# Performance work log

Measured on AMD Instinct MI355X. Metric: run time of the kernel, lower is better.

The kernel has to match this reference:

```python
import jax, jax.numpy as jnp
import numpy as np

N_NODES = 50000
N_EDGES = 800000
IN_DIM = 128
OUT_DIM = 128
NUM_RELS = 100
NUM_BASES = 4


def setup_inputs() -> dict:
    key = jax.random.key(0)
    ks = jax.random.split(key, 8)
    h = jax.random.normal(ks[0], (N_NODES, IN_DIM), dtype=jnp.float32)
    norm = jax.random.uniform(ks[1], (N_NODES, 1), dtype=jnp.float32)
    src = jax.random.randint(ks[2], (N_EDGES,), 0, N_NODES, dtype=jnp.int32)
    dst = jax.random.randint(ks[3], (N_EDGES,), 0, N_NODES, dtype=jnp.int32)
    rel_type = jax.random.randint(ks[4], (N_EDGES,), 0, NUM_RELS, dtype=jnp.int32)
    basis_weights = jax.random.normal(ks[5], (NUM_BASES, IN_DIM, OUT_DIM), dtype=jnp.float32) * (2.0 / np.sqrt(IN_DIM + OUT_DIM))
    coefficients = jax.random.normal(ks[6], (NUM_RELS, NUM_BASES), dtype=jnp.float32) * (1.0 / np.sqrt(NUM_RELS + NUM_BASES))
    loop_weight = jax.random.normal(ks[7], (IN_DIM, OUT_DIM), dtype=jnp.float32) * (2.0 / np.sqrt(IN_DIM + OUT_DIM))
    return {
        'h': h, 'norm': norm, 'src': src, 'dst': dst, 'rel_type': rel_type,
        'basis_weights': basis_weights, 'coefficients': coefficients,
        'loop_weight': loop_weight,
    }


def reference(h, norm, src, dst, rel_type, basis_weights, coefficients, loop_weight):
    # h: (N, in), norm: (N, 1), src/dst/rel_type: (E,)
    # basis_weights: (B, in, out), coefficients: (R, B), loop_weight: (in, out)
    n_nodes = h.shape[0]
    num_bases = basis_weights.shape[0]

    # self-loop message (dropout=0 -> identity)
    loop_message = h @ loop_weight  # (N, out)

    # W[r] = sum_b coeff[r, b] * basis[b]; per-edge msg_e = h[src_e] @ W[rel_e].
    # Reassociated: project nodes by each basis once, then mix per edge by
    # the relation coefficients -- identical math, avoids the (E, in, out)
    # gathered weight tensor of the original per-edge bmm.
    hb = jnp.einsum('ni,bio->bno', h, basis_weights)  # (B, N, out)
    c_e = coefficients[rel_type]  # (E, B)
    msg = c_e[:, 0, None] * hb[0][src]
    for b in range(1, num_bases):  # small fixed basis count
        msg = msg + c_e[:, b, None] * hb[b][src]  # (E, out)

    # scatter-sum aggregation to destination nodes, then norm scaling
    agg = jax.ops.segment_sum(msg, dst, num_segments=n_nodes)  # (N, out)
    node_repr = agg * norm  # _apply_func
    node_repr = node_repr + loop_message  # self-loop (bias=None)
    return jax.nn.relu(node_repr)  # activation
```

## Files before the change

### kernel.cpp

```cpp
#include <hip/hip_runtime.h>

typedef short bf16x8 __attribute__((ext_vector_type(8)));
typedef float floatx4 __attribute__((ext_vector_type(4)));
typedef float floatx2 __attribute__((ext_vector_type(2)));

typedef const __attribute__((address_space(1))) void* gas_ptr;
typedef __attribute__((address_space(3))) void* las_ptr;

#define EPB  4096
#define MAXB 6144

__device__ __forceinline__ unsigned short f2bf(float f) {
    unsigned int u = __float_as_uint(f);
    unsigned int r = u + 0x7fffu + ((u >> 16) & 1u);
    return (unsigned short)(r >> 16);
}

__device__ __forceinline__ void stage16(const void* g, void* lbase, int lane) {
#if __has_builtin(__builtin_amdgcn_global_load_lds)
    __builtin_amdgcn_global_load_lds((gas_ptr)g, (las_ptr)lbase, 16, 0, 0);
#else
    *(float4*)((char*)lbase + lane * 16) = *(const float4*)g;
#endif
}

__global__ __launch_bounds__(256) void prep_all(
    const float* __restrict__ h, unsigned short* __restrict__ hbf, int nconv,
    const int* __restrict__ dst, int* __restrict__ gh, int E, int nB, int nblkH,
    const float* __restrict__ basis, const float* __restrict__ loopw,
    unsigned short* __restrict__ WT2, int nb_conv)
{
    __shared__ int lh[256];
    const int b = blockIdx.x;
    const int t = threadIdx.x;
    if (b < nb_conv) {
        int idx = b * 256 + t;
        if (idx < nconv) {
            float2 v = *(const float2*)(h + (size_t)idx * 2);
            unsigned int pack = (unsigned int)f2bf(v.x) | ((unsigned int)f2bf(v.y) << 16);
            *(unsigned int*)(hbf + (size_t)idx * 2) = pack;
        }
    } else if (b < nb_conv + nblkH) {
        const int blk = b - nb_conv;
        if (t < nB) lh[t] = 0;
        __syncthreads();
        const int cbase = blk * EPB;
#pragma unroll
        for (int j = 0; j < EPB / 256; ++j) {
            int e = cbase + j * 256 + t;
            if (e < E) atomicAdd(&lh[dst[e] >> 8], 1);
        }
        __syncthreads();
        if (t < nB) gh[(size_t)t * nblkH + blk] = lh[t];
    } else {
        int c = b - nb_conv - nblkH;
        for (int k = t; k < 640; k += 256) {
            float v;
            if (k < 512) v = basis[(size_t)k * 128 + c];
            else         v = loopw[(size_t)(k - 512) * 128 + c];
            WT2[(size_t)c * 640 + k] = f2bf(v);
        }
    }
}

__global__ __launch_bounds__(256) void scan1(
    const int* __restrict__ in, int* __restrict__ bsum, int M)
{
    __shared__ int s[256];
    int i = blockIdx.x * 256 + threadIdx.x;
    int t = threadIdx.x;
    s[t] = (i < M) ? in[i] : 0;
    __syncthreads();
    for (int o = 128; o > 0; o >>= 1) {
        if (t < o) s[t] += s[t + o];
        __syncthreads();
    }
    if (t == 0) bsum[blockIdx.x] = s[0];
}

__global__ __launch_bounds__(256) void scan_final(
    const int* __restrict__ in, const int* __restrict__ bsum,
    int* __restrict__ out, int M)
{
    __shared__ int s[256];
    __shared__ int sb[256];
    int t = threadIdx.x;
    int i = blockIdx.x * 256 + t;
    sb[t] = (t < (int)blockIdx.x) ? bsum[t] : 0;
    int v = (i < M) ? in[i] : 0;
    s[t] = v;
    __syncthreads();
    for (int o = 128; o > 0; o >>= 1) {
        if (t < o) sb[t] += sb[t + o];
        __syncthreads();
    }
    for (int o = 1; o < 256; o <<= 1) {
        int x = (t >= o) ? s[t - o] : 0;
        __syncthreads();
        s[t] += x;
        __syncthreads();
    }
    if (i < M) out[i] = s[t] - v + sb[0];
}

__global__ __launch_bounds__(256) void scatter_bkt(
    const int* __restrict__ dst, const int* __restrict__ src,
    const int* __restrict__ rel, const int* __restrict__ sgh,
    unsigned int* __restrict__ tmp, int E, int nB, int nblkH)
{
    __shared__ int cur[256];
    const int blk = blockIdx.x;
    const int t = threadIdx.x;
    if (t < nB) cur[t] = sgh[(size_t)t * nblkH + blk];
    __syncthreads();
    const int cbase = blk * EPB;
#pragma unroll
    for (int j = 0; j < EPB / 256; ++j) {
        int e = cbase + j * 256 + t;
        if (e < E) {
            int d = dst[e];
            int slot = atomicAdd(&cur[d >> 8], 1);
            tmp[slot] = (unsigned int)src[e] | ((unsigned int)rel[e] << 16)
                      | ((unsigned int)(d & 255) << 23);
        }
    }
}

__global__ __launch_bounds__(256) void bucket_sort(
    const unsigned int* __restrict__ tmp, const int* __restrict__ sgh,
    unsigned int* __restrict__ sedge, int* __restrict__ rowptr,
    int E, int N, int nB, int nblkH)
{
    __shared__ unsigned int eb[MAXB];
    __shared__ int hh[256], ss[256], cur[256];
    const int b = blockIdx.x;
    const int t = threadIdx.x;
    const int brow = sgh[(size_t)b * nblkH];
    const int next = (b + 1 < nB) ? sgh[(size_t)(b + 1) * nblkH] : E;
    int n = next - brow;
    if (n > MAXB) n = MAXB;
    hh[t] = 0;
    __syncthreads();
    for (int i = t; i < n; i += 256) {
        unsigned int v = tmp[brow + i];
        eb[i] = v;
        atomicAdd(&hh[(v >> 23) & 255], 1);
    }
    __syncthreads();
    int v = hh[t];
    ss[t] = v;
    __syncthreads();
    for (int o = 1; o < 256; o <<= 1) {
        int x = (t >= o) ? ss[t - o] : 0;
        __syncthreads();
        ss[t] += x;
        __syncthreads();
    }
    const int excl = ss[t] - v;
    const int idx = b * 256 + t;
    if (idx <= N) rowptr[idx] = brow + excl;
    cur[t] = excl;
    __syncthreads();
    for (int i = t; i < n; i += 256) {
        unsigned int e = eb[i];
        int slot = atomicAdd(&cur[(e >> 23) & 255], 1);
        sedge[brow + slot] = ((e & 0xFFFFu) << 8) | (((e >> 16) & 0x7Fu) << 25);
    }
}

__global__ __launch_bounds__(256) void aggregate_pre(
    const unsigned short* __restrict__ hbf,
    const int* __restrict__ rowptr,
    const unsigned int* __restrict__ sedge,
    const float* __restrict__ coeff,
    const float* __restrict__ norm,
    unsigned short* __restrict__ A2, int N, int R)
{
    __shared__ float scoef[512];
    for (int i = threadIdx.x; i < R * 4; i += 256) scoef[i] = coeff[i];
    __syncthreads();

    const int wave = threadIdx.x >> 6;
    const int lane = threadIdx.x & 63;
    const int d = blockIdx.x * 4 + wave;
    if (d >= N) return;
    int i = rowptr[d];
    const int end = rowptr[d + 1];

    const char* hbase = (const char*)hbf + lane * 4;

    floatx2 a0 = {0.f, 0.f}, a1 = {0.f, 0.f}, a2 = {0.f, 0.f}, a3 = {0.f, 0.f};

#define EDGE_LOAD(v, u) \
    unsigned int u = *(const unsigned int*)(hbase + ((v) & 0x00FFFF00u));
#define EDGE_MATH(v, u) { \
    const float4 c = *(const float4*)((const char*)scoef + (((v) >> 25) << 4)); \
    floatx2 hp; \
    hp[0] = __uint_as_float((u) << 16); \
    hp[1] = __uint_as_float((u) & 0xFFFF0000u); \
    a0 = __builtin_elementwise_fma((floatx2){c.x, c.x}, hp, a0); \
    a1 = __builtin_elementwise_fma((floatx2){c.y, c.y}, hp, a1); \
    a2 = __builtin_elementwise_fma((floatx2){c.z, c.z}, hp, a2); \
    a3 = __builtin_elementwise_fma((floatx2){c.w, c.w}, hp, a3); }

    while (i < end && (i & 3)) {
        unsigned int v = sedge[i];
        EDGE_LOAD(v, u)
        EDGE_MATH(v, u)
        ++i;
    }
    for (; i + 8 <= end; i += 8) {
        uint4 e0 = *(const uint4*)(sedge + i);
        uint4 e1 = *(const uint4*)(sedge + i + 4);
        EDGE_LOAD(e0.x, u0) EDGE_LOAD(e0.y, u1) EDGE_LOAD(e0.z, u2) EDGE_LOAD(e0.w, u3)
        EDGE_LOAD(e1.x, u4) EDGE_LOAD(e1.y, u5) EDGE_LOAD(e1.z, u6) EDGE_LOAD(e1.w, u7)
        EDGE_MATH(e0.x, u0) EDGE_MATH(e0.y, u1) EDGE_MATH(e0.z, u2) EDGE_MATH(e0.w, u3)
        EDGE_MATH(e1.x, u4) EDGE_MATH(e1.y, u5) EDGE_MATH(e1.z, u6) EDGE_MATH(e1.w, u7)
    }
    for (; i + 4 <= end; i += 4) {
        uint4 e0 = *(const uint4*)(sedge + i);
        EDGE_LOAD(e0.x, u0) EDGE_LOAD(e0.y, u1) EDGE_LOAD(e0.z, u2) EDGE_LOAD(e0.w, u3)
        EDGE_MATH(e0.x, u0) EDGE_MATH(e0.y, u1) EDGE_MATH(e0.z, u2) EDGE_MATH(e0.w, u3)
    }
    for (; i < end; ++i) {
        unsigned int v = sedge[i];
        EDGE_LOAD(v, u)
        EDGE_MATH(v, u)
    }
#undef EDGE_LOAD
#undef EDGE_MATH

    const float nm = norm[d];
    unsigned short* row = A2 + (size_t)d * 512 + lane * 2;
    *(unsigned int*)(row)       = (unsigned int)f2bf(a0[0] * nm) | ((unsigned int)f2bf(a0[1] * nm) << 16);
    *(unsigned int*)(row + 128) = (unsigned int)f2bf(a1[0] * nm) | ((unsigned int)f2bf(a1[1] * nm) << 16);
    *(unsigned int*)(row + 256) = (unsigned int)f2bf(a2[0] * nm) | ((unsigned int)f2bf(a2[1] * nm) << 16);
    *(unsigned int*)(row + 384) = (unsigned int)f2bf(a3[0] * nm) | ((unsigned int)f2bf(a3[1] * nm) << 16);
}

__global__ __launch_bounds__(256) void final_gemm(
    const unsigned short* __restrict__ A2,
    const unsigned short* __restrict__ hbf,
    const unsigned short* __restrict__ WT2,
    float* __restrict__ out, int N)
{
    __shared__ char sA[16384];
    __shared__ char sB[16384];
    const int t = threadIdx.x;
    const int w = t >> 6;
    const int lane = t & 63;
    const int quad = lane >> 4;
    const int low  = lane & 15;
    const int wr = w >> 1, wc = w & 1;
    const int m0 = blockIdx.x * 128;

    floatx4 acc[4][4];
#pragma unroll
    for (int mt = 0; mt < 4; ++mt)
#pragma unroll
        for (int nt = 0; nt < 4; ++nt) acc[mt][nt] = (floatx4){0.f, 0.f, 0.f, 0.f};

    for (int it = 0; it < 10; ++it) {
        const int k0 = it * 64;
#pragma unroll
        for (int i = 0; i < 4; ++i) {
            const int slot = i * 256 + t;
            const int kc  = slot >> 7;
            const int idx = slot & 127;
            int grow = m0 + idx;
            if (grow >= N) grow = N - 1;
            const unsigned short* gA = (k0 < 512)
                ? A2  + (size_t)grow * 512 + k0 + kc * 8
                : hbf + (size_t)grow * 128 + (k0 - 512) + kc * 8;
            const unsigned short* gB = WT2 + (size_t)idx * 640 + k0 + kc * 8;
            stage16(gA, sA + (size_t)(i * 256 + w * 64) * 16, lane);
            stage16(gB, sB + (size_t)(i * 256 + w * 64) * 16, lane);
        }
        __syncthreads();

#pragma unroll
        for (int ks = 0; ks < 2; ++ks) {
            bf16x8 af[4], bfr[4];
#pragma unroll
            for (int mt = 0; mt < 4; ++mt)
                af[mt] = *(const bf16x8*)(sA + (size_t)(((ks * 4 + quad) << 7) + wr * 64 + mt * 16 + low) * 16);
#pragma unroll
            for (int nt = 0; nt < 4; ++nt)
                bfr[nt] = *(const bf16x8*)(sB + (size_t)(((ks * 4 + quad) << 7) + wc * 64 + nt * 16 + low) * 16);
#pragma unroll
            for (int mt = 0; mt < 4; ++mt)
#pragma unroll
                for (int nt = 0; nt < 4; ++nt)
                    acc[mt][nt] = __builtin_amdgcn_mfma_f32_16x16x32_bf16(af[mt], bfr[nt], acc[mt][nt], 0, 0, 0);
        }
        __syncthreads();
    }

#pragma unroll
    for (int mt = 0; mt < 4; ++mt) {
#pragma unroll
        for (int nt = 0; nt < 4; ++nt) {
            const int c = wc * 64 + nt * 16 + low;
#pragma unroll
            for (int r = 0; r < 4; ++r) {
                int rr = m0 + wr * 64 + mt * 16 + quad * 4 + r;
                if (rr < N) out[(size_t)rr * 128 + c] = fmaxf(acc[mt][nt][r], 0.f);
            }
        }
    }
}

extern "C" void kernel_launch(void* const* d_in, const int* in_sizes, int n_in,
                              void* d_out, int out_size, void* d_ws, size_t ws_size,
                              hipStream_t stream)
{
    const float* h     = (const float*)d_in[0];
    const float* norm  = (const float*)d_in[1];
    const int*   src   = (const int*)d_in[2];
    const int*   dst   = (const int*)d_in[3];
    const int*   rel   = (const int*)d_in[4];
    const float* basis = (const float*)d_in[5];
    const float* coeff = (const float*)d_in[6];
    const float* loopw = (const float*)d_in[7];
    float* out = (float*)d_out;

    const int N = in_sizes[1];
    const int E = in_sizes[2];
    const int R = in_sizes[6] / 4;

    const int nB    = (N + 255) >> 8;
    const int nblkH = (E + EPB - 1) / EPB;
    const int M     = nB * nblkH;
    const int NBs   = (M + 255) / 256;

    char* ws = (char*)d_ws;
    size_t off = 0;
    auto walloc = [&](size_t bytes) -> char* {
        char* p = ws + off;
        off = (off + bytes + 255) & ~(size_t)255;
        return p;
    };
    unsigned short* A2     = (unsigned short*)walloc((size_t)N * 512 * 2);
    unsigned short* hbf    = (unsigned short*)walloc((size_t)N * 128 * 2);
    unsigned short* WT2    = (unsigned short*)walloc(128 * 640 * 2);
    int*            rowptr = (int*)walloc((size_t)(N + 1) * 4);
    int*            bsum   = (int*)walloc((size_t)NBs * 4);
    int*            gh     = (int*)walloc((size_t)M * 4);
    int*            sgh    = (int*)walloc((size_t)M * 4);
    unsigned int*   tmp    = (unsigned int*)walloc((size_t)E * 4);
    unsigned int*   sedge  = (unsigned int*)walloc((size_t)E * 4);

    const int nconv = N * 64;
    const int nb_conv = (nconv + 255) / 256;

    prep_all<<<nb_conv + nblkH + 128, 256, 0, stream>>>(
        h, hbf, nconv, dst, gh, E, nB, nblkH, basis, loopw, WT2, nb_conv);
    scan1<<<NBs, 256, 0, stream>>>(gh, bsum, M);
    scan_final<<<NBs, 256, 0, stream>>>(gh, bsum, sgh, M);
    scatter_bkt<<<nblkH, 256, 0, stream>>>(dst, src, rel, sgh, tmp, E, nB, nblkH);
    bucket_sort<<<nB, 256, 0, stream>>>(tmp, sgh, sedge, rowptr, E, N, nB, nblkH);
    aggregate_pre<<<(N + 3) / 4, 256, 0, stream>>>(hbf, rowptr, sedge, coeff, norm, A2, N, R);
    final_gemm<<<(N + 127) / 128, 256, 0, stream>>>(A2, hbf, WT2, out, N);
}
```

Before: 202.1 us.

## Fuse edge aggregation with final GEMM through a swizzled LDS tile

Result: slower. 231.4 us (+14.5%).

```diff
diff --git a/kernel.cpp b/kernel.cpp
--- a/kernel.cpp
+++ b/kernel.cpp
@@ -3,9 +3,6 @@
 typedef short bf16x8 __attribute__((ext_vector_type(8)));
 typedef float floatx4 __attribute__((ext_vector_type(4)));
 typedef float floatx2 __attribute__((ext_vector_type(2)));
-
-typedef const __attribute__((address_space(1))) void* gas_ptr;
-typedef __attribute__((address_space(3))) void* las_ptr;
 
 #define EPB  4096
 #define MAXB 6144
@@ -14,14 +11,6 @@
     unsigned int u = __float_as_uint(f);
     unsigned int r = u + 0x7fffu + ((u >> 16) & 1u);
     return (unsigned short)(r >> 16);
-}
-
-__device__ __forceinline__ void stage16(const void* g, void* lbase, int lane) {
-#if __has_builtin(__builtin_amdgcn_global_load_lds)
-    __builtin_amdgcn_global_load_lds((gas_ptr)g, (las_ptr)lbase, 16, 0, 0);
-#else
-    *(float4*)((char*)lbase + lane * 16) = *(const float4*)g;
-#endif
 }
 
 __global__ __launch_bounds__(256) void prep_all(
@@ -168,28 +157,27 @@
     }
 }
 
-__global__ __launch_bounds__(256) void aggregate_pre(
+__global__ __launch_bounds__(256, 4) void agg_gemm(
     const unsigned short* __restrict__ hbf,
     const int* __restrict__ rowptr,
     const unsigned int* __restrict__ sedge,
     const float* __restrict__ coeff,
     const float* __restrict__ norm,
-    unsigned short* __restrict__ A2, int N, int R)
-{
+    const unsigned short* __restrict__ WT2,
+    float* __restrict__ out, int N, int R)
+{
+    __shared__ unsigned short sA[64 * 32 * 8];
     __shared__ float scoef[512];
-    for (int i = threadIdx.x; i < R * 4; i += 256) scoef[i] = coeff[i];
-    __syncthreads();
-
-    const int wave = threadIdx.x >> 6;
-    const int lane = threadIdx.x & 63;
-    const int d = blockIdx.x * 4 + wave;
-    if (d >= N) return;
-    int i = rowptr[d];
-    const int end = rowptr[d + 1];
+
+    const int t = threadIdx.x;
+    for (int i = t; i < R * 4; i += 256) scoef[i] = coeff[i];
+    __syncthreads();
+
+    const int wave = t >> 6;
+    const int lane = t & 63;
+    const int m0 = blockIdx.x * 32;
 
     const char* hbase = (const char*)hbf + lane * 4;
-
-    floatx2 a0 = {0.f, 0.f}, a1 = {0.f, 0.f}, a2 = {0.f, 0.f}, a3 = {0.f, 0.f};
 
 #define EDGE_LOAD(v, u) \
     unsigned int u = *(const unsigned int*)(hbase + ((v) & 0x00FFFF00u));
@@ -198,113 +186,125 @@
     floatx2 hp; \
     hp[0] = __uint_as_float((u) << 16); \
     hp[1] = __uint_as_float((u) & 0xFFFF0000u); \
-    a0 = __builtin_elementwise_fma((floatx2){c.x, c.x}, hp, a0); \
-    a1 = __builtin_elementwise_fma((floatx2){c.y, c.y}, hp, a1); \
-    a2 = __builtin_elementwise_fma((floatx2){c.z, c.z}, hp, a2); \
-    a3 = __builtin_elementwise_fma((floatx2){c.w, c.w}, hp, a3); }
-
-    while (i < end && (i & 3)) {
-        unsigned int v = sedge[i];
-        EDGE_LOAD(v, u)
-        EDGE_MATH(v, u)
-        ++i;
-    }
-    for (; i + 8 <= end; i += 8) {
-        uint4 e0 = *(const uint4*)(sedge + i);
-        uint4 e1 = *(const uint4*)(sedge + i + 4);
-        EDGE_LOAD(e0.x, u0) EDGE_LOAD(e0.y, u1) EDGE_LOAD(e0.z, u2) EDGE_LOAD(e0.w, u3)
-        EDGE_LOAD(e1.x, u4) EDGE_LOAD(e1.y, u5) EDGE_LOAD(e1.z, u6) EDGE_LOAD(e1.w, u7)
-        EDGE_MATH(e0.x, u0) EDGE_MATH(e0.y, u1) EDGE_MATH(e0.z, u2) EDGE_MATH(e0.w, u3)
-        EDGE_MATH(e1.x, u4) EDGE_MATH(e1.y, u5) EDGE_MATH(e1.z, u6) EDGE_MATH(e1.w, u7)
-    }
-    for (; i + 4 <= end; i += 4) {
-        uint4 e0 = *(const uint4*)(sedge + i);
-        EDGE_LOAD(e0.x, u0) EDGE_LOAD(e0.y, u1) EDGE_LOAD(e0.z, u2) EDGE_LOAD(e0.w, u3)
-        EDGE_MATH(e0.x, u0) EDGE_MATH(e0.y, u1) EDGE_MATH(e0.z, u2) EDGE_MATH(e0.w, u3)
-    }
-    for (; i < end; ++i) {
-        unsigned int v = sedge[i];
-        EDGE_LOAD(v, u)
-        EDGE_MATH(v, u)
+    a[0] = __builtin_elementwise_fma((floatx2){c.x, c.x}, hp, a[0]); \
+    a[1] = __builtin_elementwise_fma((floatx2){c.y, c.y}, hp, a[1]); \
+    a[2] = __builtin_elementwise_fma((floatx2){c.z, c.z}, hp, a[2]); \
+    a[3] = __builtin_elementwise_fma((floatx2){c.w, c.w}, hp, a[3]); }
+
+    for (int j = 0; j < 8; ++j) {
+        const int r = wave * 8 + j;
+        const int d = m0 + r;
+        if (d >= N) break;
+        int i = rowptr[d];
+        const int end = rowptr[d + 1];
+
+        floatx2 a[4];
+        a[0] = (floatx2){0.f, 0.f}; a[1] = (floatx2){0.f, 0.f};
+        a[2] = (floatx2){0.f, 0.f}; a[3] = (floatx2){0.f, 0.f};
+
+        while (i < end && (i & 3)) {
+            unsigned int v = sedge[i];
+            EDGE_LOAD(v, u)
+            EDGE_MATH(v, u)
+            ++i;
+        }
+        for (; i + 8 <= end; i += 8) {
+            uint4 e0 = *(const uint4*)(sedge + i);
+            uint4 e1 = *(const uint4*)(sedge + i + 4);
+            EDGE_LOAD(e0.x, u0) EDGE_LOAD(e0.y, u1) EDGE_LOAD(e0.z, u2) EDGE_LOAD(e0.w, u3)
+            EDGE_LOAD(e1.x, u4) EDGE_LOAD(e1.y, u5) EDGE_LOAD(e1.z, u6) EDGE_LOAD(e1.w, u7)
+            EDGE_MATH(e0.x, u0) EDGE_MATH(e0.y, u1) EDGE_MATH(e0.z, u2) EDGE_MATH(e0.w, u3)
+            EDGE_MATH(e1.x, u4) EDGE_MATH(e1.y, u5) EDGE_MATH(e1.z, u6) EDGE_MATH(e1.w, u7)
+        }
+        for (; i + 4 <= end; i += 4) {
+            uint4 e0 = *(const uint4*)(sedge + i);
+            EDGE_LOAD(e0.x, u0) EDGE_LOAD(e0.y, u1) EDGE_LOAD(e0.z, u2) EDGE_LOAD(e0.w, u3)
+            EDGE_MATH(e0.x, u0) EDGE_MATH(e0.y, u1) EDGE_MATH(e0.z, u2) EDGE_MATH(e0.w, u3)
+        }
+        for (; i < end; ++i) {
+            unsigned int v = sedge[i];
+            EDGE_LOAD(v, u)
+            EDGE_MATH(v, u)
+        }
+
+        const float nm = norm[d];
+        const int kbase = lane >> 2;
+        const int boff = (lane & 3) * 4;
+#pragma unroll
+        for (int b = 0; b < 4; ++b) {
+            unsigned int pack = (unsigned int)f2bf(a[b][0] * nm)
+                              | ((unsigned int)f2bf(a[b][1] * nm) << 16);
+            const int kc = b * 16 + kbase;
+            const int slot = kc * 32 + (r ^ (kc & 7));
+            *(unsigned int*)((char*)sA + (size_t)slot * 16 + boff) = pack;
+        }
     }
 #undef EDGE_LOAD
 #undef EDGE_MATH
 
-    const float nm = norm[d];
-    unsigned short* row = A2 + (size_t)d * 512 + lane * 2;
-    *(unsigned int*)(row)       = (unsigned int)f2bf(a0[0] * nm) | ((unsigned int)f2bf(a0[1] * nm) << 16);
-    *(unsigned int*)(row + 128) = (unsigned int)f2bf(a1[0] * nm) | ((unsigned int)f2bf(a1[1] * nm) << 16);
-    *(unsigned int*)(row + 256) = (unsigned int)f2bf(a2[0] * nm) | ((unsigned int)f2bf(a2[1] * nm) << 16);
-    *(unsigned int*)(row + 384) = (unsigned int)f2bf(a3[0] * nm) | ((unsigned int)f2bf(a3[1] * nm) << 16);
-}
-
-__global__ __launch_bounds__(256) void final_gemm(
-    const unsigned short* __restrict__ A2,
-    const unsigned short* __restrict__ hbf,
-    const unsigned short* __restrict__ WT2,
-    float* __restrict__ out, int N)
-{
-    __shared__ char sA[16384];
-    __shared__ char sB[16384];
-    const int t = threadIdx.x;
-    const int w = t >> 6;
-    const int lane = t & 63;
+    __syncthreads();
+
     const int quad = lane >> 4;
     const int low  = lane & 15;
-    const int wr = w >> 1, wc = w & 1;
-    const int m0 = blockIdx.x * 128;
-
-    floatx4 acc[4][4];
-#pragma unroll
-    for (int mt = 0; mt < 4; ++mt)
-#pragma unroll
-        for (int nt = 0; nt < 4; ++nt) acc[mt][nt] = (floatx4){0.f, 0.f, 0.f, 0.f};
-
-    for (int it = 0; it < 10; ++it) {
-        const int k0 = it * 64;
-#pragma unroll
-        for (int i = 0; i < 4; ++i) {
-            const int slot = i * 256 + t;
-            const int kc  = slot >> 7;
-            const int idx = slot & 127;
-            int grow = m0 + idx;
-            if (grow >= N) grow = N - 1;
-            const unsigned short* gA = (k0 < 512)
-                ? A2  + (size_t)grow * 512 + k0 + kc * 8
-                : hbf + (size_t)grow * 128 + (k0 - 512) + kc * 8;
-            const unsigned short* gB = WT2 + (size_t)idx * 640 + k0 + kc * 8;
-            stage16(gA, sA + (size_t)(i * 256 + w * 64) * 16, lane);
-            stage16(gB, sB + (size_t)(i * 256 + w * 64) * 16, lane);
-        }
-        __syncthreads();
-
-#pragma unroll
-        for (int ks = 0; ks < 2; ++ks) {
-            bf16x8 af[4], bfr[4];
-#pragma unroll
-            for (int mt = 0; mt < 4; ++mt)
-                af[mt] = *(const bf16x8*)(sA + (size_t)(((ks * 4 + quad) << 7) + wr * 64 + mt * 16 + low) * 16);
-#pragma unroll
-            for (int nt = 0; nt < 4; ++nt)
-                bfr[nt] = *(const bf16x8*)(sB + (size_t)(((ks * 4 + quad) << 7) + wc * 64 + nt * 16 + low) * 16);
-#pragma unroll
-            for (int mt = 0; mt < 4; ++mt)
-#pragma unroll
-                for (int nt = 0; nt < 4; ++nt)
-                    acc[mt][nt] = __builtin_amdgcn_mfma_f32_16x16x32_bf16(af[mt], bfr[nt], acc[mt][nt], 0, 0, 0);
-        }
-        __syncthreads();
-    }
-
-#pragma unroll
-    for (int mt = 0; mt < 4; ++mt) {
-#pragma unroll
-        for (int nt = 0; nt < 4; ++nt) {
-            const int c = wc * 64 + nt * 16 + low;
-#pragma unroll
-            for (int r = 0; r < 4; ++r) {
-                int rr = m0 + wr * 64 + mt * 16 + quad * 4 + r;
-                if (rr < N) out[(size_t)rr * 128 + c] = fmaxf(acc[mt][nt][r], 0.f);
+
+    floatx4 acc[2][2];
+#pragma unroll
+    for (int mt = 0; mt < 2; ++mt)
+#pragma unroll
+        for (int nt = 0; nt < 2; ++nt) acc[mt][nt] = (floatx4){0.f, 0.f, 0.f, 0.f};
+
+#pragma unroll 4
+    for (int kk = 0; kk < 16; ++kk) {
+        const int kcq = kk * 4 + quad;
+        bf16x8 af[2], bfr[2];
+#pragma unroll
+        for (int mt = 0; mt < 2; ++mt) {
+            const int row = mt * 16 + low;
+            af[mt] = *(const bf16x8*)((const char*)sA
+                        + (size_t)(kcq * 32 + (row ^ (kcq & 7))) * 16);
+        }
+#pragma unroll
+        for (int nt = 0; nt < 2; ++nt) {
+            const int col = wave * 32 + nt * 16 + low;
+            bfr[nt] = *(const bf16x8*)(WT2 + (size_t)col * 640 + kk * 32 + quad * 8);
+        }
+#pragma unroll
+        for (int mt = 0; mt < 2; ++mt)
+#pragma unroll
+            for (int nt = 0; nt < 2; ++nt)
+                acc[mt][nt] = __builtin_amdgcn_mfma_f32_16x16x32_bf16(af[mt], bfr[nt], acc[mt][nt], 0, 0, 0);
+    }
+
+#pragma unroll
+    for (int kk = 16; kk < 20; ++kk) {
+        bf16x8 af[2], bfr[2];
+#pragma unroll
+        for (int mt = 0; mt < 2; ++mt) {
+            int rowd = m0 + mt * 16 + low;
+            if (rowd >= N) rowd = N - 1;
+            af[mt] = *(const bf16x8*)(hbf + (size_t)rowd * 128 + (kk - 16) * 32 + quad * 8);
+        }
+#pragma unroll
+        for (int nt = 0; nt < 2; ++nt) {
+            const int col = wave * 32 + nt * 16 + low;
+            bfr[nt] = *(const bf16x8*)(WT2 + (size_t)col * 640 + kk * 32 + quad * 8);
+        }
+#pragma unroll
+        for (int mt = 0; mt < 2; ++mt)
+#pragma unroll
+            for (int nt = 0; nt < 2; ++nt)
+                acc[mt][nt] = __builtin_amdgcn_mfma_f32_16x16x32_bf16(af[mt], bfr[nt], acc[mt][nt], 0, 0, 0);
+    }
+
+#pragma unroll
+    for (int mt = 0; mt < 2; ++mt) {
+#pragma unroll
+        for (int nt = 0; nt < 2; ++nt) {
+            const int c = wave * 32 + nt * 16 + low;
+#pragma unroll
+            for (int r2 = 0; r2 < 4; ++r2) {
+                int rr = m0 + mt * 16 + quad * 4 + r2;
+                if (rr < N) out[(size_t)rr * 128 + c] = fmaxf(acc[mt][nt][r2], 0.f);
             }
         }
     }
@@ -340,7 +340,6 @@
         off = (off + bytes + 255) & ~(size_t)255;
         return p;
     };
-    unsigned short* A2     = (unsigned short*)walloc((size_t)N * 512 * 2);
     unsigned short* hbf    = (unsigned short*)walloc((size_t)N * 128 * 2);
     unsigned short* WT2    = (unsigned short*)walloc(128 * 640 * 2);
     int*            rowptr = (int*)walloc((size_t)(N + 1) * 4);
@@ -359,6 +358,5 @@
     scan_final<<<NBs, 256, 0, stream>>>(gh, bsum, sgh, M);
     scatter_bkt<<<nblkH, 256, 0, stream>>>(dst, src, rel, sgh, tmp, E, nB, nblkH);
     bucket_sort<<<nB, 256, 0, stream>>>(tmp, sgh, sedge, rowptr, E, N, nB, nblkH);
-    aggregate_pre<<<(N + 3) / 4, 256, 0, stream>>>(hbf, rowptr, sedge, coeff, norm, A2, N, R);
-    final_gemm<<<(N + 127) / 128, 256, 0, stream>>>(A2, hbf, WT2, out, N);
-}
+    agg_gemm<<<(N + 31) / 32, 256, 0, stream>>>(hbf, rowptr, sedge, coeff, norm, WT2, out, N, R);
+}
```

## Replace bucketed two-pass CSR sort with direct global-atomic counting sort

Applied to the files above, without the earlier changes.

Result: slower. 259.3 us (+28.3%).

```diff
diff --git a/kernel.cpp b/kernel.cpp
--- a/kernel.cpp
+++ b/kernel.cpp
@@ -6,9 +6,6 @@
 
 typedef const __attribute__((address_space(1))) void* gas_ptr;
 typedef __attribute__((address_space(3))) void* las_ptr;
-
-#define EPB  4096
-#define MAXB 6144
 
 __device__ __forceinline__ unsigned short f2bf(float f) {
     unsigned int u = __float_as_uint(f);
@@ -25,35 +22,35 @@
 }
 
 __global__ __launch_bounds__(256) void prep_all(
-    const float* __restrict__ h, unsigned short* __restrict__ hbf, int nconv,
-    const int* __restrict__ dst, int* __restrict__ gh, int E, int nB, int nblkH,
+    const float* __restrict__ h, unsigned short* __restrict__ hbf, int nconv8,
+    const int* __restrict__ dst, int* __restrict__ cnt, int E, int nhist,
     const float* __restrict__ basis, const float* __restrict__ loopw,
     unsigned short* __restrict__ WT2, int nb_conv)
 {
-    __shared__ int lh[256];
     const int b = blockIdx.x;
     const int t = threadIdx.x;
     if (b < nb_conv) {
         int idx = b * 256 + t;
-        if (idx < nconv) {
-            float2 v = *(const float2*)(h + (size_t)idx * 2);
-            unsigned int pack = (unsigned int)f2bf(v.x) | ((unsigned int)f2bf(v.y) << 16);
-            *(unsigned int*)(hbf + (size_t)idx * 2) = pack;
-        }
-    } else if (b < nb_conv + nblkH) {
+        if (idx < nconv8) {
+            const float4 v0 = *(const float4*)(h + (size_t)idx * 8);
+            const float4 v1 = *(const float4*)(h + (size_t)idx * 8 + 4);
+            uint4 p;
+            p.x = (unsigned int)f2bf(v0.x) | ((unsigned int)f2bf(v0.y) << 16);
+            p.y = (unsigned int)f2bf(v0.z) | ((unsigned int)f2bf(v0.w) << 16);
+            p.z = (unsigned int)f2bf(v1.x) | ((unsigned int)f2bf(v1.y) << 16);
+            p.w = (unsigned int)f2bf(v1.z) | ((unsigned int)f2bf(v1.w) << 16);
+            *(uint4*)(hbf + (size_t)idx * 8) = p;
+        }
+    } else if (b < nb_conv + nhist) {
         const int blk = b - nb_conv;
-        if (t < nB) lh[t] = 0;
-        __syncthreads();
-        const int cbase = blk * EPB;
-#pragma unroll
-        for (int j = 0; j < EPB / 256; ++j) {
+        const int cbase = blk * 2048;
+#pragma unroll
+        for (int j = 0; j < 8; ++j) {
             int e = cbase + j * 256 + t;
-            if (e < E) atomicAdd(&lh[dst[e] >> 8], 1);
-        }
-        __syncthreads();
-        if (t < nB) gh[(size_t)t * nblkH + blk] = lh[t];
+            if (e < E) atomicAdd(&cnt[dst[e]], 1);
+        }
     } else {
-        int c = b - nb_conv - nblkH;
+        int c = b - nb_conv - nhist;
         for (int k = t; k < 640; k += 256) {
             float v;
             if (k < 512) v = basis[(size_t)k * 128 + c];
@@ -80,7 +77,7 @@
 
 __global__ __launch_bounds__(256) void scan_final(
     const int* __restrict__ in, const int* __restrict__ bsum,
-    int* __restrict__ out, int M)
+    int* __restrict__ rowptr, int* __restrict__ gcur, int M, int E)
 {
     __shared__ int s[256];
     __shared__ int sb[256];
@@ -100,71 +97,29 @@
         s[t] += x;
         __syncthreads();
     }
-    if (i < M) out[i] = s[t] - v + sb[0];
-}
-
-__global__ __launch_bounds__(256) void scatter_bkt(
+    if (i < M) {
+        int excl = s[t] - v + sb[0];
+        rowptr[i] = excl;
+        gcur[i]   = excl;
+    }
+    if (blockIdx.x == 0 && t == 0) rowptr[M] = E;
+}
+
+__global__ __launch_bounds__(256) void scatter_direct(
     const int* __restrict__ dst, const int* __restrict__ src,
-    const int* __restrict__ rel, const int* __restrict__ sgh,
-    unsigned int* __restrict__ tmp, int E, int nB, int nblkH)
-{
-    __shared__ int cur[256];
-    const int blk = blockIdx.x;
+    const int* __restrict__ rel, int* __restrict__ gcur,
+    unsigned int* __restrict__ sedge, int E)
+{
+    const int cbase = blockIdx.x * 2048;
     const int t = threadIdx.x;
-    if (t < nB) cur[t] = sgh[(size_t)t * nblkH + blk];
-    __syncthreads();
-    const int cbase = blk * EPB;
-#pragma unroll
-    for (int j = 0; j < EPB / 256; ++j) {
+#pragma unroll
+    for (int j = 0; j < 8; ++j) {
         int e = cbase + j * 256 + t;
         if (e < E) {
             int d = dst[e];
-            int slot = atomicAdd(&cur[d >> 8], 1);
-            tmp[slot] = (unsigned int)src[e] | ((unsigned int)rel[e] << 16)
-                      | ((unsigned int)(d & 255) << 23);
-        }
-    }
-}
-
-__global__ __launch_bounds__(256) void bucket_sort(
-    const unsigned int* __restrict__ tmp, const int* __restrict__ sgh,
-    unsigned int* __restrict__ sedge, int* __restrict__ rowptr,
-    int E, int N, int nB, int nblkH)
-{
-    __shared__ unsigned int eb[MAXB];
-    __shared__ int hh[256], ss[256], cur[256];
-    const int b = blockIdx.x;
-    const int t = threadIdx.x;
-    const int brow = sgh[(size_t)b * nblkH];
-    const int next = (b + 1 < nB) ? sgh[(size_t)(b + 1) * nblkH] : E;
-    int n = next - brow;
-    if (n > MAXB) n = MAXB;
-    hh[t] = 0;
-    __syncthreads();
-    for (int i = t; i < n; i += 256) {
-        unsigned int v = tmp[brow + i];
-        eb[i] = v;
-        atomicAdd(&hh[(v >> 23) & 255], 1);
-    }
-    __syncthreads();
-    int v = hh[t];
-    ss[t] = v;
-    __syncthreads();
-    for (int o = 1; o < 256; o <<= 1) {
-        int x = (t >= o) ? ss[t - o] : 0;
-        __syncthreads();
-        ss[t] += x;
-        __syncthreads();
-    }
-    const int excl = ss[t] - v;
-    const int idx = b * 256 + t;
-    if (idx <= N) rowptr[idx] = brow + excl;
-    cur[t] = excl;
-    __syncthreads();
-    for (int i = t; i < n; i += 256) {
-        unsigned int e = eb[i];
-        int slot = atomicAdd(&cur[(e >> 23) & 255], 1);
-        sedge[brow + slot] = ((e & 0xFFFFu) << 8) | (((e >> 16) & 0x7Fu) << 25);
+            int slot = atomicAdd(&gcur[d], 1);
+            sedge[slot] = ((unsigned int)src[e] << 8) | ((unsigned int)rel[e] << 25);
+        }
     }
 }
 
@@ -328,10 +283,7 @@
     const int E = in_sizes[2];
     const int R = in_sizes[6] / 4;
 
-    const int nB    = (N + 255) >> 8;
-    const int nblkH = (E + EPB - 1) / EPB;
-    const int M     = nB * nblkH;
-    const int NBs   = (M + 255) / 256;
+    const int NBs = (N + 255) / 256;
 
     char* ws = (char*)d_ws;
     size_t off = 0;
@@ -344,21 +296,22 @@
     unsigned short* hbf    = (unsigned short*)walloc((size_t)N * 128 * 2);
     unsigned short* WT2    = (unsigned short*)walloc(128 * 640 * 2);
     int*            rowptr = (int*)walloc((size_t)(N + 1) * 4);
+    int*            cnt    = (int*)walloc((size_t)N * 4);
+    int*            gcur   = (int*)walloc((size_t)N * 4);
     int*            bsum   = (int*)walloc((size_t)NBs * 4);
-    int*            gh     = (int*)walloc((size_t)M * 4);
-    int*            sgh    = (int*)walloc((size_t)M * 4);
-    unsigned int*   tmp    = (unsigned int*)walloc((size_t)E * 4);
     unsigned int*   sedge  = (unsigned int*)walloc((size_t)E * 4);
 
-    const int nconv = N * 64;
-    const int nb_conv = (nconv + 255) / 256;
-
-    prep_all<<<nb_conv + nblkH + 128, 256, 0, stream>>>(
-        h, hbf, nconv, dst, gh, E, nB, nblkH, basis, loopw, WT2, nb_conv);
-    scan1<<<NBs, 256, 0, stream>>>(gh, bsum, M);
-    scan_final<<<NBs, 256, 0, stream>>>(gh, bsum, sgh, M);
-    scatter_bkt<<<nblkH, 256, 0, stream>>>(dst, src, rel, sgh, tmp, E, nB, nblkH);
-    bucket_sort<<<nB, 256, 0, stream>>>(tmp, sgh, sedge, rowptr, E, N, nB, nblkH);
+    const int nconv8  = N * 16;
+    const int nb_conv = (nconv8 + 255) / 256;
+    const int nhist   = (E + 2047) / 2048;
+    const int nscat   = (E + 2047) / 2048;
+
+    hipMemsetAsync(cnt, 0, (size_t)N * 4, stream);
+    prep_all<<<nb_conv + nhist + 128, 256, 0, stream>>>(
+        h, hbf, nconv8, dst, cnt, E, nhist, basis, loopw, WT2, nb_conv);
+    scan1<<<NBs, 256, 0, stream>>>(cnt, bsum, N);
+    scan_final<<<NBs, 256, 0, stream>>>(cnt, bsum, rowptr, gcur, N, E);
+    scatter_direct<<<nscat, 256, 0, stream>>>(dst, src, rel, gcur, sedge, E);
     aggregate_pre<<<(N + 3) / 4, 256, 0, stream>>>(hbf, rowptr, sedge, coeff, norm, A2, N, R);
     final_gemm<<<(N + 127) / 128, 256, 0, stream>>>(A2, hbf, WT2, out, N);
 }
```
